# Performance work log

Measured on AMD Instinct MI355X. Metric: run time of the kernel, lower is better.

Reference implementation:

```python
import jax, jax.numpy as jnp
import numpy as np

D_MODEL = 256
NUM_UNIVERSES = 8
D_UNIVERSE = D_MODEL // NUM_UNIVERSES
B, S = 1, 1024
TEMP = 5.0
NEG = -1e9


def setup_inputs() -> dict:
    key = jax.random.key(0)
    ks = jax.random.split(key, 5)
    scale = 1.0 / np.sqrt(D_MODEL)
    return {
        "x": jax.random.normal(ks[0], (B, S, D_MODEL), dtype=jnp.float32),
        "Wq": jax.random.normal(ks[1], (D_MODEL, D_MODEL), dtype=jnp.float32) * scale,
        "bq": jnp.zeros((D_MODEL,), dtype=jnp.float32),
        "Wk": jax.random.normal(ks[2], (D_MODEL, D_MODEL), dtype=jnp.float32) * scale,
        "bk": jnp.zeros((D_MODEL,), dtype=jnp.float32),
        "Wv": jax.random.normal(ks[3], (D_MODEL, D_MODEL), dtype=jnp.float32) * scale,
        "bv": jnp.zeros((D_MODEL,), dtype=jnp.float32),
        "Wo": jax.random.normal(ks[4], (D_MODEL, D_MODEL), dtype=jnp.float32) * scale,
        "bo": jnp.zeros((D_MODEL,), dtype=jnp.float32),
    }


def reference(x, Wq, bq, Wk, bk, Wv, bv, Wo, bo):
    b, s, d = x.shape
    h, du = NUM_UNIVERSES, D_UNIVERSE
    # Projections; Q,K squashed to [0,1] fuzzy truth values
    Q = jax.nn.sigmoid(x @ Wq + bq)
    K = jax.nn.sigmoid(x @ Wk + bk)
    V = x @ Wv + bv
    # [B,S,D] -> [B,H,S,du]
    Q = Q.reshape(b, s, h, du).transpose(0, 2, 1, 3)
    K = K.reshape(b, s, h, du).transpose(0, 2, 1, 3)
    V = V.reshape(b, s, h, du).transpose(0, 2, 1, 3)
    # Fuzzy implication: clamp(1 - Q_i + K_j, max=1), mean over d_universe
    # Broadcast to [B,H,S,S,du] (the memory-heavy intermediate)
    implication = jnp.minimum(1.0 - Q[:, :, :, None, :] + K[:, :, None, :, :], 1.0)
    truth = implication.mean(axis=-1)  # [B,H,S,S]
    # Causal mask
    causal = jnp.tril(jnp.ones((s, s), dtype=bool))
    truth = jnp.where(causal[None, None], truth, NEG)
    attn = jax.nn.softmax(truth * TEMP, axis=-1)
    out = jnp.einsum("bhij,bhjd->bhid", attn, V)
    out = out.transpose(0, 2, 1, 3).reshape(b, s, d)
    return out @ Wo + bo
```

## Files before the change

kernel.cpp:

```cpp
#include <hip/hip_runtime.h>
#include <math.h>

#define S_LEN 1024
#define DM    256
#define DU    32
#define TEMPF 5.0f
#define NS    4

__global__ __launch_bounds__(256) void qkv_proj_kernel(
    const float* __restrict__ x,
    const float* __restrict__ Wq, const float* __restrict__ bq,
    const float* __restrict__ Wk, const float* __restrict__ bk,
    const float* __restrict__ Wv, const float* __restrict__ bv,
    float* __restrict__ qo, float* __restrict__ ko, float* __restrict__ vo)
{
    const int mat = blockIdx.z;
    const float* __restrict__ W    = (mat == 0) ? Wq : ((mat == 1) ? Wk : Wv);
    const float* __restrict__ bias = (mat == 0) ? bq : ((mat == 1) ? bk : bv);
    float* __restrict__ dst        = (mat == 0) ? qo : ((mat == 1) ? ko : vo);

    const int n0 = blockIdx.x * 64;
    const int m0 = blockIdx.y * 32;
    const int t  = threadIdx.x;
    const int tx = t & 15;
    const int ty = t >> 4;

    __shared__ float xs[2][32][36];
    __shared__ float wsh[2][32][68];

    float acc[2][4] = {};

    const int xrow = t & 31;
    const int xkc  = (t >> 5) * 4;
    const int wrow = t >> 4;
    const int wcol = (t & 15) * 4;

    float4 xa = *(const float4*)&x[(m0 + xrow) * DM + xkc];
    float4 wa = *(const float4*)&W[wrow * DM + n0 + wcol];
    float4 wb = *(const float4*)&W[(wrow + 16) * DM + n0 + wcol];
    xs[0][xkc + 0][xrow] = xa.x; xs[0][xkc + 1][xrow] = xa.y;
    xs[0][xkc + 2][xrow] = xa.z; xs[0][xkc + 3][xrow] = xa.w;
    *(float4*)&wsh[0][wrow][wcol]      = wa;
    *(float4*)&wsh[0][wrow + 16][wcol] = wb;
    __syncthreads();

    int cur = 0;
    for (int k0 = 32; k0 < DM; k0 += 32) {
        xa = *(const float4*)&x[(m0 + xrow) * DM + k0 + xkc];
        wa = *(const float4*)&W[(k0 + wrow) * DM + n0 + wcol];
        wb = *(const float4*)&W[(k0 + wrow + 16) * DM + n0 + wcol];
        #pragma unroll
        for (int kk = 0; kk < 32; kk++) {
            float2 a2 = *(const float2*)&xs[cur][kk][ty * 2];
            float4 b4 = *(const float4*)&wsh[cur][kk][tx * 4];
            acc[0][0] += a2.x * b4.x; acc[0][1] += a2.x * b4.y;
            acc[0][2] += a2.x * b4.z; acc[0][3] += a2.x * b4.w;
            acc[1][0] += a2.y * b4.x; acc[1][1] += a2.y * b4.y;
            acc[1][2] += a2.y * b4.z; acc[1][3] += a2.y * b4.w;
        }
        const int nxt = cur ^ 1;
        xs[nxt][xkc + 0][xrow] = xa.x; xs[nxt][xkc + 1][xrow] = xa.y;
        xs[nxt][xkc + 2][xrow] = xa.z; xs[nxt][xkc + 3][xrow] = xa.w;
        *(float4*)&wsh[nxt][wrow][wcol]      = wa;
        *(float4*)&wsh[nxt][wrow + 16][wcol] = wb;
        __syncthreads();
        cur = nxt;
    }
    #pragma unroll
    for (int kk = 0; kk < 32; kk++) {
        float2 a2 = *(const float2*)&xs[cur][kk][ty * 2];
        float4 b4 = *(const float4*)&wsh[cur][kk][tx * 4];
        acc[0][0] += a2.x * b4.x; acc[0][1] += a2.x * b4.y;
        acc[0][2] += a2.x * b4.z; acc[0][3] += a2.x * b4.w;
        acc[1][0] += a2.y * b4.x; acc[1][1] += a2.y * b4.y;
        acc[1][2] += a2.y * b4.z; acc[1][3] += a2.y * b4.w;
    }

    #pragma unroll
    for (int j = 0; j < 4; j++) {
        const int cidx = n0 + tx * 4 + j;
        const float bb = bias[cidx];
        const int hh = cidx >> 5;
        const int dd = cidx & 31;
        #pragma unroll
        for (int i = 0; i < 2; i++) {
            const int row = m0 + ty * 2 + i;
            float val = acc[i][j] + bb;
            if (mat < 2) val = 1.0f / (1.0f + __expf(-val));
            dst[hh * (S_LEN * DU) + row * DU + dd] = val;
        }
    }
}

__global__ __launch_bounds__(256, 2) void attn_kernel(
    const float* __restrict__ q, const float* __restrict__ k,
    const float* __restrict__ v,
    float* __restrict__ part_o, float* __restrict__ part_l)
{
    const int bid = blockIdx.x;
    const int it4 = 15 - (bid >> 5);
    const int sub = bid & 31;
    const int h   = sub & 7;
    const int s   = sub >> 3;
    const int t   = threadIdx.x;
    const int r   = t >> 4;
    const int c   = t & 15;
    const int i0  = it4 * 64;

    __shared__ float  Ks[64][36];
    __shared__ float4 Vs4[16][2][17];
    __shared__ float  Ps[64][68];

    float qreg[4][32];
    #pragma unroll
    for (int kq = 0; kq < 4; kq++) {
        const float* qrow = q + h * (S_LEN * DU) + (i0 + r + 16 * kq) * DU;
        #pragma unroll
        for (int d4 = 0; d4 < 8; d4++) {
            float4 qv = *(const float4*)&qrow[d4 * 4];
            qreg[kq][d4*4+0] = qv.x; qreg[kq][d4*4+1] = qv.y;
            qreg[kq][d4*4+2] = qv.z; qreg[kq][d4*4+3] = qv.w;
        }
    }

    float o0[4] = {0,0,0,0}, o1[4] = {0,0,0,0}, lpart[4] = {0,0,0,0};

    const int jr = t >> 2;
    const int d0 = (t & 3) * 8;
    const float* kbase = k + h * (S_LEN * DU);
    const float* vbase = v + h * (S_LEN * DU);

    const int njt = it4 + 1;
    float4 ka, kb, va, vb;
    if (s < njt) {
        const float* kp = kbase + (s * 64 + jr) * DU + d0;
        const float* vp = vbase + (s * 64 + jr) * DU + d0;
        ka = *(const float4*)kp; kb = *(const float4*)(kp + 4);
        va = *(const float4*)vp; vb = *(const float4*)(vp + 4);
    }

    for (int jt = s; jt < njt; jt += NS) {
        __syncthreads();
        *(float4*)&Ks[jr][d0]     = ka;
        *(float4*)&Ks[jr][d0 + 4] = kb;
        {
            float vv[8] = {va.x, va.y, va.z, va.w, vb.x, vb.y, vb.z, vb.w};
            #pragma unroll
            for (int i = 0; i < 8; i++) {
                const int d = d0 + i;
                ((float*)&Vs4[jr >> 2][d >> 4][d & 15])[jr & 3] = vv[i];
            }
        }
        __syncthreads();
        if (jt + NS < njt) {
            const float* kp = kbase + ((jt + NS) * 64 + jr) * DU + d0;
            const float* vp = vbase + ((jt + NS) * 64 + jr) * DU + d0;
            ka = *(const float4*)kp; kb = *(const float4*)(kp + 4);
            va = *(const float4*)vp; vb = *(const float4*)(vp + 4);
        }

        #pragma unroll
        for (int q4 = 0; q4 < 4; q4++) {
            const int jj  = c + q4 * 16;
            const int jgl = jt * 64 + jj;
            float sacc[4] = {0,0,0,0};
            #pragma unroll
            for (int d = 0; d < 32; d += 4) {
                float4 k4 = *(const float4*)&Ks[jj][d];
                #pragma unroll
                for (int kq = 0; kq < 4; kq++) {
                    sacc[kq] += fmaxf(qreg[kq][d+0] - k4.x, 0.0f)
                              + fmaxf(qreg[kq][d+1] - k4.y, 0.0f)
                              + fmaxf(qreg[kq][d+2] - k4.z, 0.0f)
                              + fmaxf(qreg[kq][d+3] - k4.w, 0.0f);
                }
            }
            #pragma unroll
            for (int kq = 0; kq < 4; kq++) {
                const int ig = i0 + r + 16 * kq;
                const float p = (jgl <= ig)
                    ? __expf(TEMPF - (TEMPF / 32.0f) * sacc[kq]) : 0.0f;
                lpart[kq] += p;
                Ps[r + 16 * kq][jj] = p;
            }
        }

        #pragma unroll 4
        for (int j4 = 0; j4 < 16; j4++) {
            float4 vA = Vs4[j4][0][c];
            float4 vB = Vs4[j4][1][c];
            #pragma unroll
            for (int kq = 0; kq < 4; kq++) {
                float4 pj = *(const float4*)&Ps[r + 16 * kq][j4 * 4];
                o0[kq] += pj.x*vA.x + pj.y*vA.y + pj.z*vA.z + pj.w*vA.w;
                o1[kq] += pj.x*vB.x + pj.y*vB.y + pj.z*vB.z + pj.w*vB.w;
            }
        }
    }

    #pragma unroll
    for (int off = 8; off; off >>= 1)
        #pragma unroll
        for (int kq = 0; kq < 4; kq++)
            lpart[kq] += __shfl_xor(lpart[kq], off, 16);

    const int pbase = (h * 16 + it4) * NS + s;
    float* po = part_o + pbase * 2048;
    #pragma unroll
    for (int kq = 0; kq < 4; kq++) {
        po[(r + 16 * kq) * 32 + c]      = o0[kq];
        po[(r + 16 * kq) * 32 + c + 16] = o1[kq];
    }
    if (c == 0) {
        #pragma unroll
        for (int kq = 0; kq < 4; kq++)
            part_l[pbase * 64 + r + 16 * kq] = lpart[kq];
    }
}

__global__ __launch_bounds__(256) void combine_kernel(
    const float* __restrict__ part_o, const float* __restrict__ part_l,
    float* __restrict__ attn)
{
    const int h    = blockIdx.x & 7;
    const int it4  = blockIdx.x >> 3;
    const int t    = threadIdx.x;
    const int r    = t >> 4;
    const int c    = t & 15;
    const int base = (h * 16 + it4) * NS;

    #pragma unroll
    for (int kq = 0; kq < 4; kq++) {
        const int row = r + 16 * kq;
        float os0 = 0.0f, os1 = 0.0f, ls = 0.0f;
        #pragma unroll
        for (int s2 = 0; s2 < NS; s2++) {
            const float* po = part_o + (base + s2) * 2048;
            os0 += po[row * 32 + c];
            os1 += po[row * 32 + c + 16];
            ls  += part_l[(base + s2) * 64 + row];
        }
        const float inv = 1.0f / ls;
        attn[(it4 * 64 + row) * DM + h * DU + c]      = os0 * inv;
        attn[(it4 * 64 + row) * DM + h * DU + c + 16] = os1 * inv;
    }
}

__global__ __launch_bounds__(256) void out_proj_kernel(
    const float* __restrict__ a, const float* __restrict__ W,
    const float* __restrict__ bias, float* __restrict__ dst)
{
    const int n0 = blockIdx.x * 32;
    const int m0 = blockIdx.y * 32;
    const int t  = threadIdx.x;
    const int tx = t & 15;
    const int ty = t >> 4;

    __shared__ float xs[2][32][36];
    __shared__ float wsh[2][32][36];

    float acc[2][2] = {};

    const int arow = t & 31;
    const int akc  = (t >> 5) * 4;
    const int wr   = t >> 3;
    const int wc   = (t & 7) * 4;

    float4 xa = *(const float4*)&a[(m0 + arow) * DM + akc];
    float4 wa = *(const float4*)&W[wr * DM + n0 + wc];
    xs[0][akc + 0][arow] = xa.x; xs[0][akc + 1][arow] = xa.y;
    xs[0][akc + 2][arow] = xa.z; xs[0][akc + 3][arow] = xa.w;
    *(float4*)&wsh[0][wr][wc] = wa;
    __syncthreads();

    int cur = 0;
    for (int k0 = 32; k0 < DM; k0 += 32) {
        xa = *(const float4*)&a[(m0 + arow) * DM + k0 + akc];
        wa = *(const float4*)&W[(k0 + wr) * DM + n0 + wc];
        #pragma unroll
        for (int kk = 0; kk < 32; kk++) {
            float2 a2 = *(const float2*)&xs[cur][kk][ty * 2];
            float2 b2 = *(const float2*)&wsh[cur][kk][tx * 2];
            acc[0][0] += a2.x * b2.x; acc[0][1] += a2.x * b2.y;
            acc[1][0] += a2.y * b2.x; acc[1][1] += a2.y * b2.y;
        }
        const int nxt = cur ^ 1;
        xs[nxt][akc + 0][arow] = xa.x; xs[nxt][akc + 1][arow] = xa.y;
        xs[nxt][akc + 2][arow] = xa.z; xs[nxt][akc + 3][arow] = xa.w;
        *(float4*)&wsh[nxt][wr][wc] = wa;
        __syncthreads();
        cur = nxt;
    }
    #pragma unroll
    for (int kk = 0; kk < 32; kk++) {
        float2 a2 = *(const float2*)&xs[cur][kk][ty * 2];
        float2 b2 = *(const float2*)&wsh[cur][kk][tx * 2];
        acc[0][0] += a2.x * b2.x; acc[0][1] += a2.x * b2.y;
        acc[1][0] += a2.y * b2.x; acc[1][1] += a2.y * b2.y;
    }

    #pragma unroll
    for (int j = 0; j < 2; j++) {
        const int cidx = n0 + tx * 2 + j;
        const float bb = bias[cidx];
        #pragma unroll
        for (int i = 0; i < 2; i++) {
            const int row = m0 + ty * 2 + i;
            dst[row * DM + cidx] = acc[i][j] + bb;
        }
    }
}

extern "C" void kernel_launch(void* const* d_in, const int* in_sizes, int n_in,
                              void* d_out, int out_size, void* d_ws, size_t ws_size,
                              hipStream_t stream)
{
    const float* x  = (const float*)d_in[0];
    const float* Wq = (const float*)d_in[1];
    const float* bq = (const float*)d_in[2];
    const float* Wk = (const float*)d_in[3];
    const float* bk = (const float*)d_in[4];
    const float* Wv = (const float*)d_in[5];
    const float* bv = (const float*)d_in[6];
    const float* Wo = (const float*)d_in[7];
    const float* bo = (const float*)d_in[8];
    float* out = (float*)d_out;

    float* ws      = (float*)d_ws;
    float* q       = ws;
    float* k       = q + 262144;
    float* v       = k + 262144;
    float* attn    = v + 262144;
    float* part_o  = attn + 262144;
    float* part_l  = part_o + 1048576;

    qkv_proj_kernel<<<dim3(4, 32, 3), 256, 0, stream>>>(x, Wq, bq, Wk, bk, Wv, bv, q, k, v);
    attn_kernel<<<dim3(512), 256, 0, stream>>>(q, k, v, part_o, part_l);
    combine_kernel<<<dim3(128), 256, 0, stream>>>(part_o, part_l, attn);
    out_proj_kernel<<<dim3(8, 32), 256, 0, stream>>>(attn, Wo, bo, out);
}
```

Before: 118.6 us.

## Split attention into one block per causal tile pair and use bf16 MFMA for PV

```diff
diff --git a/kernel.cpp b/kernel.cpp
--- a/kernel.cpp
+++ b/kernel.cpp
@@ -1,11 +1,20 @@
 #include <hip/hip_runtime.h>
+#include <hip/hip_bf16.h>
 #include <math.h>
 
 #define S_LEN 1024
 #define DM    256
 #define DU    32
 #define TEMPF 5.0f
-#define NS    4
+
+typedef float f32x4  __attribute__((ext_vector_type(4)));
+typedef short bf16x8 __attribute__((ext_vector_type(8)));
+
+__device__ __forceinline__ unsigned short f32_to_bf16_rne(float x) {
+    unsigned int b = __float_as_uint(x);
+    b += 0x7FFFu + ((b >> 16) & 1u);
+    return (unsigned short)(b >> 16);
+}
 
 __global__ __launch_bounds__(256) void qkv_proj_kernel(
     const float* __restrict__ x,
@@ -98,18 +107,22 @@
     float* __restrict__ part_o, float* __restrict__ part_l)
 {
     const int bid = blockIdx.x;
-    const int it4 = 15 - (bid >> 5);
-    const int sub = bid & 31;
-    const int h   = sub & 7;
-    const int s   = sub >> 3;
-    const int t   = threadIdx.x;
-    const int r   = t >> 4;
-    const int c   = t & 15;
-    const int i0  = it4 * 64;
-
-    __shared__ float  Ks[64][36];
-    __shared__ float4 Vs4[16][2][17];
-    __shared__ float  Ps[64][68];
+    const int h   = bid / 136;
+    const int rem = bid - h * 136;
+    int it4 = (int)((sqrtf(8.0f * (float)rem + 1.0f) - 1.0f) * 0.5f);
+    while ((it4 + 1) * (it4 + 2) / 2 <= rem) it4++;
+    while (it4 * (it4 + 1) / 2 > rem) it4--;
+    const int jt = rem - it4 * (it4 + 1) / 2;
+    const int i0 = it4 * 64;
+
+    const int t = threadIdx.x;
+    const int r = t >> 4;
+    const int c = t & 15;
+    const int w = t >> 6;
+
+    __shared__ __align__(16) float          Ks[64][36];
+    __shared__ __align__(16) unsigned short Vt[32][88];
+    __shared__ __align__(16) unsigned short Ps[64][88];
 
     float qreg[4][32];
     #pragma unroll
@@ -123,98 +136,80 @@
         }
     }
 
-    float o0[4] = {0,0,0,0}, o1[4] = {0,0,0,0}, lpart[4] = {0,0,0,0};
-
-    const int jr = t >> 2;
-    const int d0 = (t & 3) * 8;
-    const float* kbase = k + h * (S_LEN * DU);
-    const float* vbase = v + h * (S_LEN * DU);
-
-    const int njt = it4 + 1;
-    float4 ka, kb, va, vb;
-    if (s < njt) {
-        const float* kp = kbase + (s * 64 + jr) * DU + d0;
-        const float* vp = vbase + (s * 64 + jr) * DU + d0;
-        ka = *(const float4*)kp; kb = *(const float4*)(kp + 4);
-        va = *(const float4*)vp; vb = *(const float4*)(vp + 4);
-    }
-
-    for (int jt = s; jt < njt; jt += NS) {
-        __syncthreads();
+    {
+        const int jr = t >> 2;
+        const int d0 = (t & 3) * 8;
+        const float* kp = k + h * (S_LEN * DU) + (jt * 64 + jr) * DU + d0;
+        const float* vp = v + h * (S_LEN * DU) + (jt * 64 + jr) * DU + d0;
+        float4 ka = *(const float4*)kp, kb = *(const float4*)(kp + 4);
+        float4 va = *(const float4*)vp, vb = *(const float4*)(vp + 4);
         *(float4*)&Ks[jr][d0]     = ka;
         *(float4*)&Ks[jr][d0 + 4] = kb;
-        {
-            float vv[8] = {va.x, va.y, va.z, va.w, vb.x, vb.y, vb.z, vb.w};
-            #pragma unroll
-            for (int i = 0; i < 8; i++) {
-                const int d = d0 + i;
-                ((float*)&Vs4[jr >> 2][d >> 4][d & 15])[jr & 3] = vv[i];
-            }
-        }
-        __syncthreads();
-        if (jt + NS < njt) {
-            const float* kp = kbase + ((jt + NS) * 64 + jr) * DU + d0;
-            const float* vp = vbase + ((jt + NS) * 64 + jr) * DU + d0;
-            ka = *(const float4*)kp; kb = *(const float4*)(kp + 4);
-            va = *(const float4*)vp; vb = *(const float4*)(vp + 4);
-        }
-
-        #pragma unroll
-        for (int q4 = 0; q4 < 4; q4++) {
-            const int jj  = c + q4 * 16;
-            const int jgl = jt * 64 + jj;
-            float sacc[4] = {0,0,0,0};
-            #pragma unroll
-            for (int d = 0; d < 32; d += 4) {
-                float4 k4 = *(const float4*)&Ks[jj][d];
-                #pragma unroll
-                for (int kq = 0; kq < 4; kq++) {
-                    sacc[kq] += fmaxf(qreg[kq][d+0] - k4.x, 0.0f)
-                              + fmaxf(qreg[kq][d+1] - k4.y, 0.0f)
-                              + fmaxf(qreg[kq][d+2] - k4.z, 0.0f)
-                              + fmaxf(qreg[kq][d+3] - k4.w, 0.0f);
-                }
-            }
+        float vv[8] = {va.x, va.y, va.z, va.w, vb.x, vb.y, vb.z, vb.w};
+        #pragma unroll
+        for (int i = 0; i < 8; i++)
+            Vt[d0 + i][jr] = f32_to_bf16_rne(vv[i]);
+    }
+    __syncthreads();
+
+    float lpart[4] = {0.0f, 0.0f, 0.0f, 0.0f};
+    #pragma unroll
+    for (int q4 = 0; q4 < 4; q4++) {
+        const int jj  = c + q4 * 16;
+        const int jgl = jt * 64 + jj;
+        float sacc[4] = {0.0f, 0.0f, 0.0f, 0.0f};
+        #pragma unroll
+        for (int d = 0; d < 32; d += 4) {
+            float4 k4 = *(const float4*)&Ks[jj][d];
             #pragma unroll
             for (int kq = 0; kq < 4; kq++) {
-                const int ig = i0 + r + 16 * kq;
-                const float p = (jgl <= ig)
-                    ? __expf(TEMPF - (TEMPF / 32.0f) * sacc[kq]) : 0.0f;
-                lpart[kq] += p;
-                Ps[r + 16 * kq][jj] = p;
+                sacc[kq] += fmaxf(qreg[kq][d+0] - k4.x, 0.0f)
+                          + fmaxf(qreg[kq][d+1] - k4.y, 0.0f)
+                          + fmaxf(qreg[kq][d+2] - k4.z, 0.0f)
+                          + fmaxf(qreg[kq][d+3] - k4.w, 0.0f);
             }
         }
-
-        #pragma unroll 4
-        for (int j4 = 0; j4 < 16; j4++) {
-            float4 vA = Vs4[j4][0][c];
-            float4 vB = Vs4[j4][1][c];
-            #pragma unroll
-            for (int kq = 0; kq < 4; kq++) {
-                float4 pj = *(const float4*)&Ps[r + 16 * kq][j4 * 4];
-                o0[kq] += pj.x*vA.x + pj.y*vA.y + pj.z*vA.z + pj.w*vA.w;
-                o1[kq] += pj.x*vB.x + pj.y*vB.y + pj.z*vB.z + pj.w*vB.w;
-            }
-        }
-    }
-
+        #pragma unroll
+        for (int kq = 0; kq < 4; kq++) {
+            const int ig = i0 + r + 16 * kq;
+            const float p = (jgl <= ig)
+                ? __expf(TEMPF - (TEMPF / 32.0f) * sacc[kq]) : 0.0f;
+            lpart[kq] += p;
+            Ps[r + 16 * kq][jj] = f32_to_bf16_rne(p);
+        }
+    }
     #pragma unroll
     for (int off = 8; off; off >>= 1)
         #pragma unroll
         for (int kq = 0; kq < 4; kq++)
             lpart[kq] += __shfl_xor(lpart[kq], off, 16);
-
-    const int pbase = (h * 16 + it4) * NS + s;
-    float* po = part_o + pbase * 2048;
-    #pragma unroll
-    for (int kq = 0; kq < 4; kq++) {
-        po[(r + 16 * kq) * 32 + c]      = o0[kq];
-        po[(r + 16 * kq) * 32 + c + 16] = o1[kq];
+    __syncthreads();
+
+    const int lane = t & 63;
+    const int m    = lane & 15;
+    const int quad = lane >> 4;
+    f32x4 acc0 = {0.0f, 0.0f, 0.0f, 0.0f};
+    f32x4 acc1 = {0.0f, 0.0f, 0.0f, 0.0f};
+    #pragma unroll
+    for (int kc = 0; kc < 2; kc++) {
+        bf16x8 a  = *(const bf16x8*)&Ps[16 * w + m][kc * 32 + quad * 8];
+        bf16x8 b0 = *(const bf16x8*)&Vt[m]     [kc * 32 + quad * 8];
+        bf16x8 b1 = *(const bf16x8*)&Vt[m + 16][kc * 32 + quad * 8];
+        acc0 = __builtin_amdgcn_mfma_f32_16x16x32_bf16(a, b0, acc0, 0, 0, 0);
+        acc1 = __builtin_amdgcn_mfma_f32_16x16x32_bf16(a, b1, acc1, 0, 0, 0);
+    }
+
+    float* po = part_o + (size_t)bid * 2048;
+    #pragma unroll
+    for (int reg = 0; reg < 4; reg++) {
+        const int row = 16 * w + quad * 4 + reg;
+        po[row * 32 + m]      = acc0[reg];
+        po[row * 32 + m + 16] = acc1[reg];
     }
     if (c == 0) {
         #pragma unroll
         for (int kq = 0; kq < 4; kq++)
-            part_l[pbase * 64 + r + 16 * kq] = lpart[kq];
+            part_l[bid * 64 + r + 16 * kq] = lpart[kq];
     }
 }
 
@@ -222,27 +217,27 @@
     const float* __restrict__ part_o, const float* __restrict__ part_l,
     float* __restrict__ attn)
 {
-    const int h    = blockIdx.x & 7;
-    const int it4  = blockIdx.x >> 3;
-    const int t    = threadIdx.x;
-    const int r    = t >> 4;
-    const int c    = t & 15;
-    const int base = (h * 16 + it4) * NS;
-
-    #pragma unroll
-    for (int kq = 0; kq < 4; kq++) {
-        const int row = r + 16 * kq;
-        float os0 = 0.0f, os1 = 0.0f, ls = 0.0f;
-        #pragma unroll
-        for (int s2 = 0; s2 < NS; s2++) {
-            const float* po = part_o + (base + s2) * 2048;
-            os0 += po[row * 32 + c];
-            os1 += po[row * 32 + c + 16];
-            ls  += part_l[(base + s2) * 64 + row];
-        }
-        const float inv = 1.0f / ls;
-        attn[(it4 * 64 + row) * DM + h * DU + c]      = os0 * inv;
-        attn[(it4 * 64 + row) * DM + h * DU + c + 16] = os1 * inv;
+    const int h   = blockIdx.x & 7;
+    const int it4 = blockIdx.x >> 3;
+    const int t0  = h * 136 + it4 * (it4 + 1) / 2;
+    const int cnt = it4 + 1;
+    const int t   = threadIdx.x;
+
+    #pragma unroll
+    for (int ss = 0; ss < 2; ss++) {
+        const int slot = t * 2 + ss;
+        const int row  = slot >> 3;
+        const int d4   = (slot & 7) * 4;
+        float4 o = make_float4(0.f, 0.f, 0.f, 0.f);
+        float  l = 0.0f;
+        for (int j = 0; j < cnt; j++) {
+            float4 p = *(const float4*)&part_o[(size_t)(t0 + j) * 2048 + row * 32 + d4];
+            o.x += p.x; o.y += p.y; o.z += p.z; o.w += p.w;
+            l += part_l[(t0 + j) * 64 + row];
+        }
+        const float inv = 1.0f / l;
+        float4 res = make_float4(o.x * inv, o.y * inv, o.z * inv, o.w * inv);
+        *(float4*)&attn[(it4 * 64 + row) * DM + h * 32 + d4] = res;
     }
 }
 
@@ -332,10 +327,10 @@
     float* v       = k + 262144;
     float* attn    = v + 262144;
     float* part_o  = attn + 262144;
-    float* part_l  = part_o + 1048576;
+    float* part_l  = part_o + 2228224;
 
     qkv_proj_kernel<<<dim3(4, 32, 3), 256, 0, stream>>>(x, Wq, bq, Wk, bk, Wv, bv, q, k, v);
-    attn_kernel<<<dim3(512), 256, 0, stream>>>(q, k, v, part_o, part_l);
+    attn_kernel<<<dim3(1088), 256, 0, stream>>>(q, k, v, part_o, part_l);
     combine_kernel<<<dim3(128), 256, 0, stream>>>(part_o, part_l, attn);
     out_proj_kernel<<<dim3(8, 32), 256, 0, stream>>>(attn, Wo, bo, out);
 }
```

Result: slower. 123.2 us (+3.9%).
